# Performance work log

Hardware: AMD Instinct MI355X
Metric: run time of the kernel (lower is better)

## Reference

```python
import jax, jax.numpy as jnp
import numpy as np

B, T, C, F, E, K = 4, 2048, 1024, 4096, 8, 2
CAP_FACTOR = 1.0
AUX_COEF = 0.01
CAPACITY = max(1, int(CAP_FACTOR * (B * T) * max(1, K) / E + 0.9999))


def setup_inputs() -> dict:
    key = jax.random.key(0)
    ks = jax.random.split(key, 4)
    s = 0.02
    return {
        "x": jax.random.normal(ks[0], (B, T, C), jnp.float32),
        "w_gate": jax.random.normal(ks[1], (C, E), jnp.float32) * s,
        "b_gate": jnp.zeros((E,), jnp.float32),
        "W1": jax.random.normal(ks[2], (E, C, F), jnp.float32) * s,
        "b1": jnp.zeros((E, F), jnp.float32),
        "W2": jax.random.normal(ks[3], (E, F, C), jnp.float32) * s,
        "b2": jnp.zeros((E, C), jnp.float32),
    }


def reference(x, w_gate, b_gate, W1, b1, W2, b2):
    Bb, Tt, Cc = x.shape
    N = Bb * Tt
    S = N * K  # dispatch slots, token-major with k inner (matches the python double loop order)
    x_flat = x.reshape(N, Cc)

    # Top-K gating
    logits = x_flat @ w_gate + b_gate                       # [N, E]
    probs = jax.nn.softmax(logits, axis=-1)
    topk_w, topk_idx = jax.lax.top_k(probs, K)              # [N, K]
    topk_w = topk_w / (topk_w.sum(-1, keepdims=True) + 1e-9)

    e_flat = topk_idx.reshape(S)                            # expert id per slot
    w_flat = topk_w.reshape(S)
    tok = jnp.arange(S) // K                                # source token per slot

    # First-come-first-served capacity: position of each slot within its expert
    onehot = jax.nn.one_hot(e_flat, E, dtype=jnp.int32)     # [S, E]
    pos_in_e = (jnp.cumsum(onehot, axis=0) - onehot)        # exclusive count per expert
    pos_in_e = (pos_in_e * onehot).sum(-1)                  # [S]
    keep = pos_in_e < CAPACITY
    keepf = keep.astype(x.dtype)
    p_safe = jnp.where(keep, pos_in_e, CAPACITY - 1)        # dropped slots scatter zeros

    # Dispatch -> [E, capacity, C]
    disp = jnp.zeros((E, CAPACITY, Cc), x.dtype).at[e_flat, p_safe].add(
        x_flat[tok] * keepf[:, None]
    )

    # Per-expert FFN (grouped GEMM)
    h = jax.nn.gelu(jnp.einsum("epc,ecf->epf", disp, W1) + b1[:, None, :])
    y = jnp.einsum("epf,efc->epc", h, W2) + b2[:, None, :]  # [E, capacity, C]

    # Combine: gather each kept slot's expert output, weight, scatter-add back to tokens
    y_slot = y[e_flat, p_safe] * (w_flat * keepf)[:, None]  # [S, C]
    out = jnp.zeros((N, Cc), x.dtype).at[tok].add(y_slot).reshape(Bb, Tt, Cc)

    # Load-balancing aux loss (expert_load is detached in the original)
    expert_load = jnp.sum(onehot.astype(jnp.float32) * keepf[:, None], axis=0)  # [E]
    expert_load = jax.lax.stop_gradient(expert_load)
    frac_expected = probs.mean(axis=0)
    frac_expected = frac_expected / (frac_expected.sum() + 1e-9)
    frac_actual = expert_load / (expert_load.sum() + 1e-9)
    aux_loss = AUX_COEF * jnp.mean((frac_expected - frac_actual) ** 2)

    return out, aux_loss
```

## Files before the change

kernel.cpp:

```cpp
#include <hip/hip_runtime.h>
#include <hip/hip_bf16.h>
#include <math.h>


#define DEV __device__ __forceinline__

typedef __attribute__((ext_vector_type(4))) float f32x4;
typedef __attribute__((ext_vector_type(8))) short bf16x8;

constexpr int B_ = 4, T_ = 2048, C_ = 1024, F_ = 4096, E_ = 8, TOPK_ = 2;
constexpr int N_ = B_ * T_;
constexpr int S_ = N_ * TOPK_;
constexpr int CAP_ = 2048;

#define GLOAD16(G, L)                                              \
  __builtin_amdgcn_global_load_lds(                                \
      (const __attribute__((address_space(1))) void*)(G),          \
      (__attribute__((address_space(3))) void*)(L), 16, 0, 0)

DEV float gelu_tanh(float x) {
  float x3 = x * x * x;
  float u = 0.7978845608028654f * (x + 0.044715f * x3);
  return 0.5f * x * (1.0f + tanhf(u));
}


__global__ __launch_bounds__(256) void cvt_x_kernel(
    const float* __restrict__ in, __hip_bfloat16* __restrict__ out, int n4) {
  int i = blockIdx.x * 256 + threadIdx.x;
  if (i >= n4) return;
  float4 v = ((const float4*)in)[i];
  __hip_bfloat16 o[4] = {__float2bfloat16(v.x), __float2bfloat16(v.y),
                         __float2bfloat16(v.z), __float2bfloat16(v.w)};
  *(uint2*)(out + (size_t)i * 4) = *(uint2*)o;
}

__global__ __launch_bounds__(256) void transpose_cvt_kernel(
    const float* __restrict__ in, __hip_bfloat16* __restrict__ out, int R, int S) {
  __shared__ float tile[32][33];
  int e = blockIdx.z;
  int s0 = blockIdx.x * 32;
  int r0 = blockIdx.y * 32;
  int tx = threadIdx.x & 31;
  int ty = threadIdx.x >> 5;
  const float* ip = in + (size_t)e * R * S;
  __hip_bfloat16* op = out + (size_t)e * R * S;
#pragma unroll
  for (int i = 0; i < 32; i += 8)
    tile[ty + i][tx] = ip[(size_t)(r0 + ty + i) * S + s0 + tx];
  __syncthreads();
#pragma unroll
  for (int i = 0; i < 32; i += 8)
    op[(size_t)(s0 + ty + i) * R + r0 + tx] = __float2bfloat16(tile[tx][ty + i]);
}


__global__ __launch_bounds__(256) void gate_kernel(
    const float* __restrict__ x, const float* __restrict__ wg,
    const float* __restrict__ bg, int* __restrict__ slot_e,
    float* __restrict__ slot_w, float* __restrict__ probs_sum) {
  int lane = threadIdx.x & 63;
  int wv = threadIdx.x >> 6;
  int wid = blockIdx.x * 4 + wv;
  float psum[E_];
#pragma unroll
  for (int e = 0; e < E_; ++e) psum[e] = 0.f;

  for (int ti = 0; ti < 8; ++ti) {
    int t = wid * 8 + ti;
    const float* xr = x + (size_t)t * C_;
    float acc[E_];
#pragma unroll
    for (int e = 0; e < E_; ++e) acc[e] = 0.f;
    for (int c = lane; c < C_; c += 64) {
      float xv = xr[c];
      const float* wr = wg + (size_t)c * E_;
#pragma unroll
      for (int e = 0; e < E_; ++e) acc[e] += xv * wr[e];
    }
#pragma unroll
    for (int e = 0; e < E_; ++e) {
#pragma unroll
      for (int off = 32; off >= 1; off >>= 1)
        acc[e] += __shfl_xor(acc[e], off, 64);
    }
    if (lane == 0) {
      float lg[E_], p[E_];
      float mx = -1e30f;
#pragma unroll
      for (int e = 0; e < E_; ++e) { lg[e] = acc[e] + bg[e]; mx = fmaxf(mx, lg[e]); }
      float s = 0.f;
#pragma unroll
      for (int e = 0; e < E_; ++e) { p[e] = expf(lg[e] - mx); s += p[e]; }
      float inv = 1.f / s;
#pragma unroll
      for (int e = 0; e < E_; ++e) { p[e] *= inv; psum[e] += p[e]; }
      int i1 = 0; float p1 = p[0];
#pragma unroll
      for (int e = 1; e < E_; ++e) if (p[e] > p1) { p1 = p[e]; i1 = e; }
      int i2 = -1; float p2 = -1.f;
#pragma unroll
      for (int e = 0; e < E_; ++e) if (e != i1 && p[e] > p2) { p2 = p[e]; i2 = e; }
      float wden = 1.f / (p1 + p2 + 1e-9f);
      slot_e[2 * t] = i1;     slot_w[2 * t] = p1 * wden;
      slot_e[2 * t + 1] = i2; slot_w[2 * t + 1] = p2 * wden;
    }
  }
  if (lane == 0) {
#pragma unroll
    for (int e = 0; e < E_; ++e) atomicAdd(&probs_sum[e], psum[e]);
  }
}


__global__ __launch_bounds__(256) void scan_kernel(
    const int* __restrict__ slot_e, const float* __restrict__ slot_w,
    int* __restrict__ idx_list, float* __restrict__ w_list,
    const float* __restrict__ probs_sum, float* __restrict__ aux_out) {
  __shared__ int sc[256][E_];
  int tid = threadIdx.x;
  int s0 = tid * 64;
  int cnt[E_];
#pragma unroll
  for (int e = 0; e < E_; ++e) cnt[e] = 0;
  for (int j = 0; j < 64; ++j) cnt[slot_e[s0 + j]]++;
#pragma unroll
  for (int e = 0; e < E_; ++e) sc[tid][e] = cnt[e];
  __syncthreads();
  for (int off = 1; off < 256; off <<= 1) {
    int v[E_];
    bool act = (tid >= off);
    if (act) {
#pragma unroll
      for (int e = 0; e < E_; ++e) v[e] = sc[tid - off][e];
    }
    __syncthreads();
    if (act) {
#pragma unroll
      for (int e = 0; e < E_; ++e) sc[tid][e] += v[e];
    }
    __syncthreads();
  }
  int base[E_];
#pragma unroll
  for (int e = 0; e < E_; ++e) base[e] = tid ? sc[tid - 1][e] : 0;
  for (int j = 0; j < 64; ++j) {
    int s = s0 + j;
    int e = slot_e[s];
    int p = base[e]++;
    if (p < CAP_) {
      idx_list[e * CAP_ + p] = s >> 1;
      w_list[e * CAP_ + p] = slot_w[s];
    }
  }
  if (tid == 0) {
    float fe[E_], fa[E_], fs = 0.f, ls = 0.f;
#pragma unroll
    for (int e = 0; e < E_; ++e) {
      fe[e] = probs_sum[e] / (float)N_;
      fs += fe[e];
      int tot = sc[255][e];
      fa[e] = (float)(tot < CAP_ ? tot : CAP_);
      ls += fa[e];
    }
    float i1 = 1.f / (fs + 1e-9f), i2 = 1.f / (ls + 1e-9f);
    float a = 0.f;
#pragma unroll
    for (int e = 0; e < E_; ++e) {
      float d = fe[e] * i1 - fa[e] * i2;
      a += d * d;
    }
    aux_out[0] = 0.01f * a / (float)E_;
  }
}


template <int EPI, bool GATHER>
__global__ __launch_bounds__(512, 2) void gemm256(
    const __hip_bfloat16* __restrict__ Aall,
    const __hip_bfloat16* __restrict__ Ball,
    const int* __restrict__ idxl,
    const float* __restrict__ wl,
    const float* __restrict__ bias,
    void* __restrict__ Cout,
    const __hip_bfloat16* __restrict__ zrow,
    int Ndim, int Kdim, int ncol) {
  __shared__ __align__(16) __hip_bfloat16 lds[2][2][256 * 64];

  const int nwg = gridDim.x;
  const int wg = ((int)blockIdx.x & 7) * (nwg >> 3) + ((int)blockIdx.x >> 3);
  const int e = wg / (ncol * 8);
  const int rem = wg - e * (ncol * 8);
  const int x = rem >> 3, y = rem & 7;
  const int row0 = y * 256, col0 = x * 256;

  const int tid = threadIdx.x;
  const int lane = tid & 63;
  const int w = tid >> 6;
  const int wm = w >> 2, wn = w & 3;

  const int cb = ((lane & 7) * 16) ^ ((lane >> 5) << 5);
  const int rch = w * 8 + (lane >> 3);
  const __hip_bfloat16* srcA[4];
  const __hip_bfloat16* srcB[4];
  const __hip_bfloat16* Be = Ball + (size_t)e * Ndim * Kdim;
#pragma unroll
  for (int c = 0; c < 4; ++c) {
    int r = c * 64 + rch;
    if (GATHER) {
      int tok = idxl[e * CAP_ + row0 + r];
      srcA[c] = ((tok >= 0) ? Aall + (size_t)tok * Kdim : zrow) + (cb >> 1);
    } else {
      srcA[c] = Aall + ((size_t)e * CAP_ + row0 + r) * Kdim + (cb >> 1);
    }
    srcB[c] = Be + (size_t)(col0 + r) * Kdim + (cb >> 1);
  }
  const int dstoff = w * 512;

  const int sxor = (lane & 4) << 3;
  const int rA = wm * 128 + (lane & 15);
  const int rB = wn * 64 + (lane & 15);
  const int kb = (lane >> 4) * 16;

  f32x4 acc[8][4];
#pragma unroll
  for (int i = 0; i < 8; ++i)
#pragma unroll
    for (int j = 0; j < 4; ++j) acc[i][j] = (f32x4){0.f, 0.f, 0.f, 0.f};

  const int NT = Kdim >> 6;

#define STAGE_TILE(PAR, T)                                        \
  {                                                               \
    const int k0_ = (T) * 64;                                     \
    _Pragma("unroll") for (int c = 0; c < 4; ++c) {               \
      GLOAD16(srcA[c] + k0_, &lds[PAR][0][c * 4096 + dstoff]);    \
      GLOAD16(srcB[c] + k0_, &lds[PAR][1][c * 4096 + dstoff]);    \
    }                                                             \
  }

  STAGE_TILE(0, 0);
  asm volatile("s_waitcnt vmcnt(0)" ::: "memory");
  __builtin_amdgcn_sched_barrier(0);
  __builtin_amdgcn_s_barrier();
  __builtin_amdgcn_sched_barrier(0);

  for (int t = 0; t < NT; ++t) {
    const int par = t & 1;
    const char* baseA = (const char*)&lds[par][0][0];
    const char* baseB = (const char*)&lds[par][1][0];
    bf16x8 bfr[4][2];
#pragma unroll
    for (int q = 0; q < 4; ++q) {
      if (q == 0) {
#pragma unroll
        for (int n = 0; n < 4; ++n)
#pragma unroll
          for (int ks = 0; ks < 2; ++ks)
            bfr[n][ks] = *(const bf16x8*)(
                baseB + ((((rB + n * 16) * 128) + ks * 64 + kb) ^ sxor));
      }
      bf16x8 af[2][2];
#pragma unroll
      for (int i = 0; i < 2; ++i)
#pragma unroll
        for (int ks = 0; ks < 2; ++ks)
          af[i][ks] = *(const bf16x8*)(
              baseA + ((((rA + (q * 2 + i) * 16) * 128) + ks * 64 + kb) ^ sxor));
      if (q == 0 && t + 1 < NT) STAGE_TILE(par ^ 1, t + 1);
      __builtin_amdgcn_s_barrier();
      __builtin_amdgcn_s_setprio(1);
#pragma unroll
      for (int ks = 0; ks < 2; ++ks)
#pragma unroll
        for (int i = 0; i < 2; ++i)
#pragma unroll
          for (int n = 0; n < 4; ++n)
            acc[q * 2 + i][n] = __builtin_amdgcn_mfma_f32_16x16x32_bf16(
                af[i][ks], bfr[n][ks], acc[q * 2 + i][n], 0, 0, 0);
      __builtin_amdgcn_s_setprio(0);
      __builtin_amdgcn_s_barrier();
    }
    asm volatile("s_waitcnt vmcnt(0)" ::: "memory");
    __builtin_amdgcn_sched_barrier(0);
    __builtin_amdgcn_s_barrier();
    __builtin_amdgcn_sched_barrier(0);
  }
#undef STAGE_TILE

  const float* brow = bias + (size_t)e * Ndim;
  const int orow0 = row0 + wm * 128 + (lane >> 4) * 4;
  const int ocol0 = col0 + wn * 64 + (lane & 15);
  if (EPI == 0) {
    __hip_bfloat16* H = (__hip_bfloat16*)Cout + (size_t)e * CAP_ * Ndim;
#pragma unroll
    for (int mi = 0; mi < 8; ++mi)
#pragma unroll
      for (int n = 0; n < 4; ++n) {
        int cc = ocol0 + n * 16;
        float bv = brow[cc];
#pragma unroll
        for (int j = 0; j < 4; ++j) {
          int rr = orow0 + mi * 16 + j;
          H[(size_t)rr * Ndim + cc] = __float2bfloat16(gelu_tanh(acc[mi][n][j] + bv));
        }
      }
  } else {
    float* outp = (float*)Cout;
#pragma unroll
    for (int mi = 0; mi < 8; ++mi)
#pragma unroll
      for (int j = 0; j < 4; ++j) {
        int rr = orow0 + mi * 16 + j;
        int tk = idxl[e * CAP_ + rr];
        if (tk < 0) continue;
        float ww = wl[e * CAP_ + rr];
#pragma unroll
        for (int n = 0; n < 4; ++n) {
          int cc = ocol0 + n * 16;
          unsafeAtomicAdd(&outp[(size_t)tk * C_ + cc], ww * (acc[mi][n][j] + brow[cc]));
        }
      }
  }
}


extern "C" void kernel_launch(void* const* d_in, const int* in_sizes, int n_in,
                              void* d_out, int out_size, void* d_ws,
                              size_t ws_size, hipStream_t stream) {
  (void)in_sizes; (void)n_in; (void)out_size; (void)ws_size;
  const float* x = (const float*)d_in[0];
  const float* w_gate = (const float*)d_in[1];
  const float* b_gate = (const float*)d_in[2];
  const float* W1 = (const float*)d_in[3];
  const float* b1 = (const float*)d_in[4];
  const float* W2 = (const float*)d_in[5];
  const float* b2 = (const float*)d_in[6];
  float* out = (float*)d_out;

  char* p = (char*)d_ws;
  __hip_bfloat16* xb = (__hip_bfloat16*)p;
  __hip_bfloat16* W1t = (__hip_bfloat16*)(p + ((size_t)16 << 20));
  __hip_bfloat16* W2t = (__hip_bfloat16*)p;
  __hip_bfloat16* Hb = (__hip_bfloat16*)(p + ((size_t)80 << 20));
  char* meta = p + ((size_t)208 << 20);
  int* slot_e = (int*)meta;
  float* slot_w = (float*)(meta + (64 << 10));
  int* idx_list = (int*)(meta + (128 << 10));
  float* w_list = (float*)(meta + (192 << 10));
  float* probs_sum = (float*)(meta + (256 << 10));
  __hip_bfloat16* zrow = (__hip_bfloat16*)(meta + (260 << 10));

  hipMemsetAsync(idx_list, 0xFF, E_ * CAP_ * sizeof(int), stream);
  hipMemsetAsync(probs_sum, 0, E_ * sizeof(float), stream);
  hipMemsetAsync(zrow, 0, 16 << 10, stream);
  hipMemsetAsync(out, 0, (size_t)N_ * C_ * sizeof(float), stream);

  cvt_x_kernel<<<(N_ * C_ / 4 + 255) / 256, 256, 0, stream>>>(x, xb, N_ * C_ / 4);
  transpose_cvt_kernel<<<dim3(F_ / 32, C_ / 32, E_), 256, 0, stream>>>(W1, W1t, C_, F_);
  gate_kernel<<<N_ / 32, 256, 0, stream>>>(x, w_gate, b_gate, slot_e, slot_w, probs_sum);
  scan_kernel<<<1, 256, 0, stream>>>(slot_e, slot_w, idx_list, w_list, probs_sum,
                                     out + (size_t)N_ * C_);
  gemm256<0, true><<<16 * 8 * E_, 512, 0, stream>>>(
      xb, W1t, idx_list, nullptr, b1, Hb, zrow, F_, C_, 16);
  transpose_cvt_kernel<<<dim3(C_ / 32, F_ / 32, E_), 256, 0, stream>>>(W2, W2t, F_, C_);
  gemm256<1, false><<<4 * 8 * E_, 512, 0, stream>>>(
      Hb, W2t, idx_list, w_list, b2, out, zrow, C_, F_, 4);
}
```

Measured before the change: 977.9 us.

## Retile expert GEMMs to 256x128 with triple-buffered K=32 pipeline and vectorized transposes

```diff
diff --git a/kernel.cpp b/kernel.cpp
--- a/kernel.cpp
+++ b/kernel.cpp
@@ -19,9 +19,8 @@
       (__attribute__((address_space(3))) void*)(L), 16, 0, 0)
 
 DEV float gelu_tanh(float x) {
-  float x3 = x * x * x;
-  float u = 0.7978845608028654f * (x + 0.044715f * x3);
-  return 0.5f * x * (1.0f + tanhf(u));
+  float u = 0.7978845608028654f * (x + 0.044715f * x * x * x);
+  return x / (1.0f + __expf(-2.0f * u));
 }
 
 
@@ -37,21 +36,36 @@
 
 __global__ __launch_bounds__(256) void transpose_cvt_kernel(
     const float* __restrict__ in, __hip_bfloat16* __restrict__ out, int R, int S) {
-  __shared__ float tile[32][33];
-  int e = blockIdx.z;
-  int s0 = blockIdx.x * 32;
-  int r0 = blockIdx.y * 32;
-  int tx = threadIdx.x & 31;
-  int ty = threadIdx.x >> 5;
+  __shared__ float tile[64][65];
+  const int e = blockIdx.z;
+  const int s0 = blockIdx.x * 64;
+  const int r0 = blockIdx.y * 64;
+  const int tx = threadIdx.x & 15;
+  const int ty = threadIdx.x >> 4;
   const float* ip = in + (size_t)e * R * S;
   __hip_bfloat16* op = out + (size_t)e * R * S;
 #pragma unroll
-  for (int i = 0; i < 32; i += 8)
-    tile[ty + i][tx] = ip[(size_t)(r0 + ty + i) * S + s0 + tx];
+  for (int it = 0; it < 4; ++it) {
+    int r = ty + it * 16;
+    float4 v = *(const float4*)&ip[(size_t)(r0 + r) * S + s0 + tx * 4];
+    tile[r][tx * 4 + 0] = v.x;
+    tile[r][tx * 4 + 1] = v.y;
+    tile[r][tx * 4 + 2] = v.z;
+    tile[r][tx * 4 + 3] = v.w;
+  }
   __syncthreads();
 #pragma unroll
-  for (int i = 0; i < 32; i += 8)
-    op[(size_t)(s0 + ty + i) * R + r0 + tx] = __float2bfloat16(tile[tx][ty + i]);
+  for (int it = 0; it < 4; ++it) {
+    int sr = ty + it * 16;
+    ushort o[4];
+#pragma unroll
+    for (int j = 0; j < 4; ++j) {
+      union { __hip_bfloat16 b; ushort u; } cv;
+      cv.b = __float2bfloat16(tile[tx * 4 + j][sr]);
+      o[j] = cv.u;
+    }
+    *(ushort4*)&op[(size_t)(s0 + sr) * R + r0 + tx * 4] = *(ushort4*)o;
+  }
 }
 
 
@@ -176,7 +190,7 @@
 
 
 template <int EPI, bool GATHER>
-__global__ __launch_bounds__(512, 2) void gemm256(
+__global__ __launch_bounds__(512, 4) void gemm256(
     const __hip_bfloat16* __restrict__ Aall,
     const __hip_bfloat16* __restrict__ Ball,
     const int* __restrict__ idxl,
@@ -185,130 +199,114 @@
     void* __restrict__ Cout,
     const __hip_bfloat16* __restrict__ zrow,
     int Ndim, int Kdim, int ncol) {
-  __shared__ __align__(16) __hip_bfloat16 lds[2][2][256 * 64];
+  __shared__ __align__(16) __hip_bfloat16 lds[3][12288];
 
   const int nwg = gridDim.x;
   const int wg = ((int)blockIdx.x & 7) * (nwg >> 3) + ((int)blockIdx.x >> 3);
   const int e = wg / (ncol * 8);
   const int rem = wg - e * (ncol * 8);
   const int x = rem >> 3, y = rem & 7;
-  const int row0 = y * 256, col0 = x * 256;
+  const int row0 = y * 256, col0 = x * 128;
 
   const int tid = threadIdx.x;
-  const int lane = tid & 63;
+  const int l = tid & 63;
   const int w = tid >> 6;
-  const int wm = w >> 2, wn = w & 3;
-
-  const int cb = ((lane & 7) * 16) ^ ((lane >> 5) << 5);
-  const int rch = w * 8 + (lane >> 3);
-  const __hip_bfloat16* srcA[4];
-  const __hip_bfloat16* srcB[4];
+  const int wm = w >> 1, wn = w & 1;
+
+  const int rst = w * 16 + (l >> 2);
+  const int colel = (((l & 3) ^ ((l >> 3) & 3)) << 3);
   const __hip_bfloat16* Be = Ball + (size_t)e * Ndim * Kdim;
-#pragma unroll
-  for (int c = 0; c < 4; ++c) {
-    int r = c * 64 + rch;
-    if (GATHER) {
-      int tok = idxl[e * CAP_ + row0 + r];
-      srcA[c] = ((tok >= 0) ? Aall + (size_t)tok * Kdim : zrow) + (cb >> 1);
-    } else {
-      srcA[c] = Aall + ((size_t)e * CAP_ + row0 + r) * Kdim + (cb >> 1);
-    }
-    srcB[c] = Be + (size_t)(col0 + r) * Kdim + (cb >> 1);
-  }
-  const int dstoff = w * 512;
-
-  const int sxor = (lane & 4) << 3;
-  const int rA = wm * 128 + (lane & 15);
-  const int rB = wn * 64 + (lane & 15);
-  const int kb = (lane >> 4) * 16;
-
-  f32x4 acc[8][4];
-#pragma unroll
-  for (int i = 0; i < 8; ++i)
+  const __hip_bfloat16 *pA0, *pA1, *pB;
+  if (GATHER) {
+    int t0 = idxl[e * CAP_ + row0 + rst];
+    int t1 = idxl[e * CAP_ + row0 + 128 + rst];
+    pA0 = ((t0 >= 0) ? Aall + (size_t)t0 * Kdim : zrow) + colel;
+    pA1 = ((t1 >= 0) ? Aall + (size_t)t1 * Kdim : zrow) + colel;
+  } else {
+    pA0 = Aall + ((size_t)e * CAP_ + row0 + rst) * Kdim + colel;
+    pA1 = Aall + ((size_t)e * CAP_ + row0 + 128 + rst) * Kdim + colel;
+  }
+  pB = Be + (size_t)(col0 + rst) * Kdim + colel;
+  const int dA0 = w * 512;
+  const int dA1 = 4096 + w * 512;
+  const int dB = 8192 + w * 512;
+
+  const int loff = (l & 15) * 64 + ((((l >> 4) ^ ((l >> 1) & 3))) << 4);
+  const int rAoff = (wm * 64) * 64 + loff;
+  const int rBoff = 8192 * 2 + (wn * 64) * 64 + loff;
+
+  f32x4 acc[4][4];
+#pragma unroll
+  for (int i = 0; i < 4; ++i)
 #pragma unroll
     for (int j = 0; j < 4; ++j) acc[i][j] = (f32x4){0.f, 0.f, 0.f, 0.f};
 
-  const int NT = Kdim >> 6;
-
-#define STAGE_TILE(PAR, T)                                        \
-  {                                                               \
-    const int k0_ = (T) * 64;                                     \
-    _Pragma("unroll") for (int c = 0; c < 4; ++c) {               \
-      GLOAD16(srcA[c] + k0_, &lds[PAR][0][c * 4096 + dstoff]);    \
-      GLOAD16(srcB[c] + k0_, &lds[PAR][1][c * 4096 + dstoff]);    \
-    }                                                             \
-  }
-
-  STAGE_TILE(0, 0);
-  asm volatile("s_waitcnt vmcnt(0)" ::: "memory");
+  const int NT = Kdim >> 5;
+
+#define STAGE(BUF)                                   \
+  {                                                  \
+    GLOAD16(pB, &lds[BUF][dB]);                      \
+    GLOAD16(pA0, &lds[BUF][dA0]);                    \
+    GLOAD16(pA1, &lds[BUF][dA1]);                    \
+    pA0 += 32; pA1 += 32; pB += 32;                  \
+  }
+
+  STAGE(0);
+  STAGE(1);
+  asm volatile("s_waitcnt vmcnt(3)" ::: "memory");
   __builtin_amdgcn_sched_barrier(0);
   __builtin_amdgcn_s_barrier();
-  __builtin_amdgcn_sched_barrier(0);
-
+
+  int par = 0;
   for (int t = 0; t < NT; ++t) {
-    const int par = t & 1;
-    const char* baseA = (const char*)&lds[par][0][0];
-    const char* baseB = (const char*)&lds[par][1][0];
-    bf16x8 bfr[4][2];
-#pragma unroll
-    for (int q = 0; q < 4; ++q) {
-      if (q == 0) {
-#pragma unroll
-        for (int n = 0; n < 4; ++n)
-#pragma unroll
-          for (int ks = 0; ks < 2; ++ks)
-            bfr[n][ks] = *(const bf16x8*)(
-                baseB + ((((rB + n * 16) * 128) + ks * 64 + kb) ^ sxor));
-      }
-      bf16x8 af[2][2];
-#pragma unroll
-      for (int i = 0; i < 2; ++i)
-#pragma unroll
-        for (int ks = 0; ks < 2; ++ks)
-          af[i][ks] = *(const bf16x8*)(
-              baseA + ((((rA + (q * 2 + i) * 16) * 128) + ks * 64 + kb) ^ sxor));
-      if (q == 0 && t + 1 < NT) STAGE_TILE(par ^ 1, t + 1);
-      __builtin_amdgcn_s_barrier();
-      __builtin_amdgcn_s_setprio(1);
-#pragma unroll
-      for (int ks = 0; ks < 2; ++ks)
-#pragma unroll
-        for (int i = 0; i < 2; ++i)
-#pragma unroll
-          for (int n = 0; n < 4; ++n)
-            acc[q * 2 + i][n] = __builtin_amdgcn_mfma_f32_16x16x32_bf16(
-                af[i][ks], bfr[n][ks], acc[q * 2 + i][n], 0, 0, 0);
-      __builtin_amdgcn_s_setprio(0);
-      __builtin_amdgcn_s_barrier();
-    }
-    asm volatile("s_waitcnt vmcnt(0)" ::: "memory");
+    const bool pre = (t + 2 < NT);
+    const int stg = (par + 2 >= 3) ? par - 1 : par + 2;
+    if (pre) STAGE(stg);
+    const char* base = (const char*)&lds[par][0];
+    bf16x8 bf[4], af[4];
+#pragma unroll
+    for (int ni = 0; ni < 4; ++ni)
+      bf[ni] = *(const bf16x8*)(base + rBoff + ni * 1024);
+#pragma unroll
+    for (int mi = 0; mi < 4; ++mi)
+      af[mi] = *(const bf16x8*)(base + rAoff + mi * 1024);
+    __builtin_amdgcn_s_setprio(1);
+#pragma unroll
+    for (int mi = 0; mi < 4; ++mi)
+#pragma unroll
+      for (int ni = 0; ni < 4; ++ni)
+        acc[mi][ni] = __builtin_amdgcn_mfma_f32_16x16x32_bf16(
+            af[mi], bf[ni], acc[mi][ni], 0, 0, 0);
+    __builtin_amdgcn_s_setprio(0);
+    if (pre) asm volatile("s_waitcnt vmcnt(3)" ::: "memory");
+    else     asm volatile("s_waitcnt vmcnt(0)" ::: "memory");
     __builtin_amdgcn_sched_barrier(0);
     __builtin_amdgcn_s_barrier();
-    __builtin_amdgcn_sched_barrier(0);
-  }
-#undef STAGE_TILE
+    par = (par + 1 >= 3) ? 0 : par + 1;
+  }
+#undef STAGE
 
   const float* brow = bias + (size_t)e * Ndim;
-  const int orow0 = row0 + wm * 128 + (lane >> 4) * 4;
-  const int ocol0 = col0 + wn * 64 + (lane & 15);
+  const int orow0 = row0 + wm * 64 + (l >> 4) * 4;
+  const int ocol0 = col0 + wn * 64 + (l & 15);
   if (EPI == 0) {
     __hip_bfloat16* H = (__hip_bfloat16*)Cout + (size_t)e * CAP_ * Ndim;
 #pragma unroll
-    for (int mi = 0; mi < 8; ++mi)
-#pragma unroll
-      for (int n = 0; n < 4; ++n) {
-        int cc = ocol0 + n * 16;
+    for (int mi = 0; mi < 4; ++mi)
+#pragma unroll
+      for (int ni = 0; ni < 4; ++ni) {
+        int cc = ocol0 + ni * 16;
         float bv = brow[cc];
 #pragma unroll
         for (int j = 0; j < 4; ++j) {
           int rr = orow0 + mi * 16 + j;
-          H[(size_t)rr * Ndim + cc] = __float2bfloat16(gelu_tanh(acc[mi][n][j] + bv));
+          H[(size_t)rr * Ndim + cc] = __float2bfloat16(gelu_tanh(acc[mi][ni][j] + bv));
         }
       }
   } else {
     float* outp = (float*)Cout;
 #pragma unroll
-    for (int mi = 0; mi < 8; ++mi)
+    for (int mi = 0; mi < 4; ++mi)
 #pragma unroll
       for (int j = 0; j < 4; ++j) {
         int rr = orow0 + mi * 16 + j;
@@ -316,9 +314,9 @@
         if (tk < 0) continue;
         float ww = wl[e * CAP_ + rr];
 #pragma unroll
-        for (int n = 0; n < 4; ++n) {
-          int cc = ocol0 + n * 16;
-          unsafeAtomicAdd(&outp[(size_t)tk * C_ + cc], ww * (acc[mi][n][j] + brow[cc]));
+        for (int ni = 0; ni < 4; ++ni) {
+          int cc = ocol0 + ni * 16;
+          unsafeAtomicAdd(&outp[(size_t)tk * C_ + cc], ww * (acc[mi][ni][j] + brow[cc]));
         }
       }
   }
@@ -357,13 +355,13 @@
   hipMemsetAsync(out, 0, (size_t)N_ * C_ * sizeof(float), stream);
 
   cvt_x_kernel<<<(N_ * C_ / 4 + 255) / 256, 256, 0, stream>>>(x, xb, N_ * C_ / 4);
-  transpose_cvt_kernel<<<dim3(F_ / 32, C_ / 32, E_), 256, 0, stream>>>(W1, W1t, C_, F_);
+  transpose_cvt_kernel<<<dim3(F_ / 64, C_ / 64, E_), 256, 0, stream>>>(W1, W1t, C_, F_);
   gate_kernel<<<N_ / 32, 256, 0, stream>>>(x, w_gate, b_gate, slot_e, slot_w, probs_sum);
   scan_kernel<<<1, 256, 0, stream>>>(slot_e, slot_w, idx_list, w_list, probs_sum,
                                      out + (size_t)N_ * C_);
-  gemm256<0, true><<<16 * 8 * E_, 512, 0, stream>>>(
-      xb, W1t, idx_list, nullptr, b1, Hb, zrow, F_, C_, 16);
-  transpose_cvt_kernel<<<dim3(C_ / 32, F_ / 32, E_), 256, 0, stream>>>(W2, W2t, F_, C_);
-  gemm256<1, false><<<4 * 8 * E_, 512, 0, stream>>>(
-      Hb, W2t, idx_list, w_list, b2, out, zrow, C_, F_, 4);
-}
+  gemm256<0, true><<<E_ * 32 * 8, 512, 0, stream>>>(
+      xb, W1t, idx_list, nullptr, b1, Hb, zrow, F_, C_, 32);
+  transpose_cvt_kernel<<<dim3(C_ / 64, F_ / 64, E_), 256, 0, stream>>>(W2, W2t, F_, C_);
+  gemm256<1, false><<<E_ * 8 * 8, 512, 0, stream>>>(
+      Hb, W2t, idx_list, w_list, b2, out, zrow, C_, F_, 8);
+}
```

Result: faster. 895.8 us (-8.4%).
